# Kernel tuning notes

Hardware: AMD Instinct MI355X
Metric: run time of the kernel (lower is better)

Reference implementation:

```python
import jax, jax.numpy as jnp
import numpy as np

ALPHA_BASE = 1.2
ALPHA_SCALE = 0.3
GRAPH_LAMBDA = 0.3
FUSION_BETA = 0.1
PRIOR_BETA = 0.2
LN_EPS = 1e-5  # nn.LayerNorm default

B, L, C = 8, 8192, 512
STAT, HID, GF, EMB = 4, 16, 16, 16


def _linear_params(key, out_d, in_d):
    kw, kb = jax.random.split(key)
    bound = 1.0 / np.sqrt(in_d)
    W = jax.random.uniform(kw, (out_d, in_d), minval=-bound, maxval=bound, dtype=jnp.float32)
    b = jax.random.uniform(kb, (out_d,), minval=-bound, maxval=bound, dtype=jnp.float32)
    return W, b


def setup_inputs() -> dict:
    key = jax.random.key(0)
    ks = jax.random.split(key, 9)
    residual = jax.random.normal(ks[0], (B, L, C), dtype=jnp.float32)
    node_embedding = jax.random.normal(ks[1], (C, EMB), dtype=jnp.float32) * 0.02
    W_l1, b_l1 = _linear_params(ks[2], HID, STAT)
    W_l2, b_l2 = _linear_params(ks[3], HID, HID)
    W_g, b_g = _linear_params(ks[4], HID, STAT)
    W_q, b_q = _linear_params(ks[5], GF, STAT)
    W_k, b_k = _linear_params(ks[6], GF, STAT)
    W_f, b_f = _linear_params(ks[7], HID, HID)
    W_o, b_o = _linear_params(ks[8], 1, HID)
    ln_g = jnp.ones((HID,), jnp.float32)
    ln_b = jnp.zeros((HID,), jnp.float32)
    return dict(residual=residual, node_embedding=node_embedding,
                W_l1=W_l1, b_l1=b_l1, W_l2=W_l2, b_l2=b_l2,
                W_g=W_g, b_g=b_g, W_q=W_q, b_q=b_q, W_k=W_k, b_k=b_k,
                W_f=W_f, b_f=b_f, W_o=W_o, b_o=b_o, ln_g=ln_g, ln_b=ln_b)


def reference(residual, node_embedding, W_l1, b_l1, W_l2, b_l2, W_g, b_g,
              W_q, b_q, W_k, b_k, W_f, b_f, W_o, b_o, ln_g, ln_b):
    # --- residual statistics: [B,L,C] -> [B,C,4] ---
    abs_res = jnp.abs(residual)
    m = abs_res.mean(axis=1)                       # mean(|r|)
    mx = abs_res.max(axis=1)                       # max(|r|)
    sq = (residual * residual).mean(axis=1)        # energy == mean(|r|^2)
    std = jnp.sqrt(jnp.maximum(sq - m * m, 0.0))   # biased std of |r|
    h0 = jnp.stack([m, mx, std, sq], axis=-1)      # [B,C,4]

    # --- local branch ---
    h_local = jax.nn.relu(h0 @ W_l1.T + b_l1) @ W_l2.T + b_l2  # [B,C,H]

    # --- adaptive adjacency ---
    q = h0 @ W_q.T + b_q                            # [B,C,G]
    k = h0 @ W_k.T + b_k                            # [B,C,G]
    sim_data = jax.nn.relu(jnp.einsum('bcg,bdg->bcd', q, k))
    sim_prior = jax.nn.relu(node_embedding @ node_embedding.T)  # [C,C]
    eye = jnp.eye(sim_data.shape[-1], dtype=sim_data.dtype)
    sim = sim_data + PRIOR_BETA * sim_prior[None] + eye[None]
    A = jax.nn.softmax(sim, axis=-1)                # [B,C,C]

    # --- message passing ---
    h_graph_in = h0 @ W_g.T + b_g                   # [B,C,H]
    msg = jnp.einsum('bcd,bdh->bch', A, h_graph_in)
    h_graph = h_graph_in + GRAPH_LAMBDA * jax.nn.relu(msg)

    # --- fusion + layernorm + head ---
    h = h_local + FUSION_BETA * h_graph
    mu = h.mean(axis=-1, keepdims=True)
    var = ((h - mu) ** 2).mean(axis=-1, keepdims=True)
    h = (h - mu) / jnp.sqrt(var + LN_EPS) * ln_g + ln_b
    h = jax.nn.relu(h @ W_f.T + b_f)
    delta = ALPHA_SCALE * jnp.tanh(h @ W_o.T + b_o)  # [B,C,1]
    alpha = (ALPHA_BASE + delta).transpose(0, 2, 1)  # [B,1,C]
    return alpha, h0, A
```

## Files before the change

kernel.cpp:

```cpp
#include <hip/hip_runtime.h>
#include <math.h>

#define BB 8
#define LL 8192
#define CC 512
#define NCH 64

#define H0_OFF (BB*CC)
#define A_OFF  (H0_OFF + BB*CC*4)

#define F_ALPHA_BASE 1.2f
#define F_ALPHA_SCALE 0.3f
#define F_GRAPH_LAMBDA 0.3f
#define F_FUSION_BETA 0.1f
#define F_PRIOR_BETA 0.2f
#define F_LN_EPS 1e-5f

struct P {
    const float* res; const float* ne;
    const float* Wl1; const float* bl1; const float* Wl2; const float* bl2;
    const float* Wg;  const float* bg;  const float* Wq;  const float* bq;
    const float* Wk;  const float* bk;  const float* Wf;  const float* bf;
    const float* Wo;  const float* bo;  const float* lng; const float* lnb;
    float* out; float* pbuf; float* h0ws;
};

__global__ __launch_bounds__(256) void k_stats(P p) {
    __shared__ float smem[3 * CC];
    int b = blockIdx.x >> 6, cb = blockIdx.x & 63;
    int sub = threadIdx.x >> 7;
    int c4 = (threadIdx.x & 127) * 4;
    const float* base = p.res + ((size_t)b * LL + cb * 128 + sub * 64) * CC + c4;
    float s0 = 0.f, s1 = 0.f, s2 = 0.f, s3 = 0.f;
    float m0 = 0.f, m1 = 0.f, m2 = 0.f, m3 = 0.f;
    float q0 = 0.f, q1 = 0.f, q2 = 0.f, q3 = 0.f;
    #pragma unroll 8
    for (int r = 0; r < 64; r++) {
        float4 v = *(const float4*)(base + (size_t)r * CC);
        s0 += fabsf(v.x); s1 += fabsf(v.y); s2 += fabsf(v.z); s3 += fabsf(v.w);
        m0 = fmaxf(m0, fabsf(v.x)); m1 = fmaxf(m1, fabsf(v.y));
        m2 = fmaxf(m2, fabsf(v.z)); m3 = fmaxf(m3, fabsf(v.w));
        q0 = fmaf(v.x, v.x, q0); q1 = fmaf(v.y, v.y, q1);
        q2 = fmaf(v.z, v.z, q2); q3 = fmaf(v.w, v.w, q3);
    }
    if (sub == 1) {
        *(float4*)&smem[0 * CC + c4] = make_float4(s0, s1, s2, s3);
        *(float4*)&smem[1 * CC + c4] = make_float4(m0, m1, m2, m3);
        *(float4*)&smem[2 * CC + c4] = make_float4(q0, q1, q2, q3);
    }
    __syncthreads();
    if (sub == 0) {
        float4 cs = *(const float4*)&smem[0 * CC + c4];
        float4 cm = *(const float4*)&smem[1 * CC + c4];
        float4 cq = *(const float4*)&smem[2 * CC + c4];
        s0 += cs.x; s1 += cs.y; s2 += cs.z; s3 += cs.w;
        m0 = fmaxf(m0, cm.x); m1 = fmaxf(m1, cm.y);
        m2 = fmaxf(m2, cm.z); m3 = fmaxf(m3, cm.w);
        q0 += cq.x; q1 += cq.y; q2 += cq.z; q3 += cq.w;
        float* pb = p.pbuf + ((size_t)(b * 3) * NCH + cb) * CC + c4;
        *(float4*)(pb)                        = make_float4(s0, s1, s2, s3);
        *(float4*)(pb + (size_t)NCH * CC)     = make_float4(m0, m1, m2, m3);
        *(float4*)(pb + (size_t)2 * NCH * CC) = make_float4(q0, q1, q2, q3);
    }
}

__global__ __launch_bounds__(256) void k_red(P p) {
    __shared__ float red[4][3][64];
    int w = threadIdx.x >> 6, lane = threadIdx.x & 63;
    int b = blockIdx.x >> 3;
    int c = (blockIdx.x & 7) * 64 + lane;
    const float* pS = p.pbuf + ((size_t)(b * 3 + 0) * NCH + w * 16) * CC + c;
    const float* pM = p.pbuf + ((size_t)(b * 3 + 1) * NCH + w * 16) * CC + c;
    const float* pQ = p.pbuf + ((size_t)(b * 3 + 2) * NCH + w * 16) * CC + c;
    float sum = 0.f, mx = 0.f, sq = 0.f;
    #pragma unroll
    for (int i = 0; i < 16; i++) {
        sum += pS[(size_t)i * CC];
        mx = fmaxf(mx, pM[(size_t)i * CC]);
        sq += pQ[(size_t)i * CC];
    }
    red[w][0][lane] = sum;
    red[w][1][lane] = mx;
    red[w][2][lane] = sq;
    __syncthreads();
    if (w == 0) {
        float ts = red[0][0][lane] + red[1][0][lane] + red[2][0][lane] + red[3][0][lane];
        float tm = fmaxf(fmaxf(red[0][1][lane], red[1][1][lane]),
                         fmaxf(red[2][1][lane], red[3][1][lane]));
        float tq = red[0][2][lane] + red[1][2][lane] + red[2][2][lane] + red[3][2][lane];
        float m = ts * (1.f / LL);
        float sqm = tq * (1.f / LL);
        float sd = sqrtf(fmaxf(sqm - m * m, 0.f));
        float4 h0v = make_float4(m, tm, sd, sqm);
        size_t g = (size_t)b * CC + c;
        *(float4*)(p.h0ws + g * 4) = h0v;
        *(float4*)(p.out + H0_OFF + g * 4) = h0v;
    }
}

__global__ __launch_bounds__(256) void k_rows(P p) {
    __shared__ float pl[4 * CC];
    int tid = threadIdx.x;
    int b = blockIdx.x >> 6, rb = blockIdx.x & 63;
    int wid = tid >> 6, lane = tid & 63;
    int row0 = rb * 8 + wid * 2;

    #pragma unroll
    for (int ccy = 0; ccy < 2; ccy++) {
        int col = tid + ccy * 256;
        float4 hv = *(const float4*)(p.h0ws + ((size_t)b * CC + col) * 4);
        pl[col] = hv.x;
        pl[CC + col] = hv.y;
        pl[2 * CC + col] = hv.z;
        pl[3 * CC + col] = hv.w;
    }

    float nr[2][16];
    #pragma unroll
    for (int rr = 0; rr < 2; rr++) {
        #pragma unroll
        for (int t = 0; t < 4; t++) {
            float4 v = *(const float4*)(p.ne + (size_t)(row0 + rr) * 16 + t * 4);
            nr[rr][4 * t] = v.x; nr[rr][4 * t + 1] = v.y;
            nr[rr][4 * t + 2] = v.z; nr[rr][4 * t + 3] = v.w;
        }
    }
    float pr0[8], pr1[8];
    #pragma unroll
    for (int j = 0; j < 8; j++) {
        int col = lane + 64 * j;
        float d0 = 0.f, d1 = 0.f;
        #pragma unroll
        for (int t = 0; t < 4; t++) {
            float4 v = *(const float4*)(p.ne + (size_t)col * 16 + t * 4);
            d0 = fmaf(nr[0][4 * t], v.x, d0); d0 = fmaf(nr[0][4 * t + 1], v.y, d0);
            d0 = fmaf(nr[0][4 * t + 2], v.z, d0); d0 = fmaf(nr[0][4 * t + 3], v.w, d0);
            d1 = fmaf(nr[1][4 * t], v.x, d1); d1 = fmaf(nr[1][4 * t + 1], v.y, d1);
            d1 = fmaf(nr[1][4 * t + 2], v.z, d1); d1 = fmaf(nr[1][4 * t + 3], v.w, d1);
        }
        pr0[j] = fmaxf(d0, 0.f);
        pr1[j] = fmaxf(d1, 0.f);
    }
    __syncthreads();

    float sloc[2][4], u[2][4], c0[2];
    #pragma unroll
    for (int rr = 0; rr < 2; rr++) {
        int row = row0 + rr;
        float sv0 = pl[row], sv1 = pl[CC + row];
        float sv2 = pl[2 * CC + row], sv3 = pl[3 * CC + row];
        sloc[rr][0] = sv0; sloc[rr][1] = sv1; sloc[rr][2] = sv2; sloc[rr][3] = sv3;
        float uu0 = 0.f, uu1 = 0.f, uu2 = 0.f, uu3 = 0.f, cc = 0.f;
        #pragma unroll
        for (int i = 0; i < 16; i++) {
            float qi = p.bq[i];
            qi = fmaf(p.Wq[i * 4 + 0], sv0, qi);
            qi = fmaf(p.Wq[i * 4 + 1], sv1, qi);
            qi = fmaf(p.Wq[i * 4 + 2], sv2, qi);
            qi = fmaf(p.Wq[i * 4 + 3], sv3, qi);
            uu0 = fmaf(qi, p.Wk[i * 4 + 0], uu0);
            uu1 = fmaf(qi, p.Wk[i * 4 + 1], uu1);
            uu2 = fmaf(qi, p.Wk[i * 4 + 2], uu2);
            uu3 = fmaf(qi, p.Wk[i * 4 + 3], uu3);
            cc = fmaf(qi, p.bk[i], cc);
        }
        u[rr][0] = uu0; u[rr][1] = uu1; u[rr][2] = uu2; u[rr][3] = uu3;
        c0[rr] = cc;
    }

    float sv[2][8];
    float mx0 = -1e30f, mx1 = -1e30f;
    #pragma unroll
    for (int j = 0; j < 8; j++) {
        int col = lane + 64 * j;
        float h0c = pl[col], h1c = pl[CC + col];
        float h2c = pl[2 * CC + col], h3c = pl[3 * CC + col];
        float d0 = c0[0], d1 = c0[1];
        d0 = fmaf(u[0][0], h0c, d0); d1 = fmaf(u[1][0], h0c, d1);
        d0 = fmaf(u[0][1], h1c, d0); d1 = fmaf(u[1][1], h1c, d1);
        d0 = fmaf(u[0][2], h2c, d0); d1 = fmaf(u[1][2], h2c, d1);
        d0 = fmaf(u[0][3], h3c, d0); d1 = fmaf(u[1][3], h3c, d1);
        float v0 = fmaxf(d0, 0.f) + F_PRIOR_BETA * pr0[j] + (col == row0 ? 1.f : 0.f);
        float v1 = fmaxf(d1, 0.f) + F_PRIOR_BETA * pr1[j] + (col == row0 + 1 ? 1.f : 0.f);
        sv[0][j] = v0; sv[1][j] = v1;
        mx0 = fmaxf(mx0, v0); mx1 = fmaxf(mx1, v1);
    }
    #pragma unroll
    for (int o = 32; o; o >>= 1) {
        mx0 = fmaxf(mx0, __shfl_xor(mx0, o));
        mx1 = fmaxf(mx1, __shfl_xor(mx1, o));
    }

    float ls0 = 0.f, ls1 = 0.f;
    float T0[4] = {0.f, 0.f, 0.f, 0.f}, T1[4] = {0.f, 0.f, 0.f, 0.f};
    #pragma unroll
    for (int j = 0; j < 8; j++) {
        int col = lane + 64 * j;
        float e0 = expf(sv[0][j] - mx0);
        float e1 = expf(sv[1][j] - mx1);
        sv[0][j] = e0; sv[1][j] = e1;
        ls0 += e0; ls1 += e1;
        float h0c = pl[col], h1c = pl[CC + col];
        float h2c = pl[2 * CC + col], h3c = pl[3 * CC + col];
        T0[0] = fmaf(e0, h0c, T0[0]); T1[0] = fmaf(e1, h0c, T1[0]);
        T0[1] = fmaf(e0, h1c, T0[1]); T1[1] = fmaf(e1, h1c, T1[1]);
        T0[2] = fmaf(e0, h2c, T0[2]); T1[2] = fmaf(e1, h2c, T1[2]);
        T0[3] = fmaf(e0, h3c, T0[3]); T1[3] = fmaf(e1, h3c, T1[3]);
    }
    #pragma unroll
    for (int o = 32; o; o >>= 1) {
        ls0 += __shfl_xor(ls0, o); ls1 += __shfl_xor(ls1, o);
        T0[0] += __shfl_xor(T0[0], o); T1[0] += __shfl_xor(T1[0], o);
        T0[1] += __shfl_xor(T0[1], o); T1[1] += __shfl_xor(T1[1], o);
        T0[2] += __shfl_xor(T0[2], o); T1[2] += __shfl_xor(T1[2], o);
        T0[3] += __shfl_xor(T0[3], o); T1[3] += __shfl_xor(T1[3], o);
    }
    float inv0 = 1.f / ls0, inv1 = 1.f / ls1;

    float* arow = p.out + A_OFF + ((size_t)b * CC + row0) * CC;
    #pragma unroll
    for (int j = 0; j < 8; j++) {
        arow[lane + 64 * j]      = sv[0][j] * inv0;
        arow[CC + lane + 64 * j] = sv[1][j] * inv1;
    }

    int rr = lane >> 5;
    float inv = rr ? inv1 : inv0;
    float Ta = (rr ? T1[0] : T0[0]) * inv;
    float Tb = (rr ? T1[1] : T0[1]) * inv;
    float Tc = (rr ? T1[2] : T0[2]) * inv;
    float Td = (rr ? T1[3] : T0[3]) * inv;
    float s20 = rr ? sloc[1][0] : sloc[0][0];
    float s21 = rr ? sloc[1][1] : sloc[0][1];
    float s22 = rr ? sloc[1][2] : sloc[0][2];
    float s23 = rr ? sloc[1][3] : sloc[0][3];

    float gcomb[16];
    #pragma unroll
    for (int h = 0; h < 16; h++) {
        float w0 = p.Wg[h * 4 + 0], w1 = p.Wg[h * 4 + 1];
        float w2 = p.Wg[h * 4 + 2], w3 = p.Wg[h * 4 + 3];
        float bgh = p.bg[h];
        float hg = bgh;
        hg = fmaf(w0, s20, hg); hg = fmaf(w1, s21, hg);
        hg = fmaf(w2, s22, hg); hg = fmaf(w3, s23, hg);
        float mg = bgh;
        mg = fmaf(w0, Ta, mg); mg = fmaf(w1, Tb, mg);
        mg = fmaf(w2, Tc, mg); mg = fmaf(w3, Td, mg);
        gcomb[h] = hg + F_GRAPH_LAMBDA * fmaxf(mg, 0.f);
    }
    float t1v[16];
    #pragma unroll
    for (int i = 0; i < 16; i++) {
        float a = p.bl1[i];
        a = fmaf(p.Wl1[i * 4 + 0], s20, a);
        a = fmaf(p.Wl1[i * 4 + 1], s21, a);
        a = fmaf(p.Wl1[i * 4 + 2], s22, a);
        a = fmaf(p.Wl1[i * 4 + 3], s23, a);
        t1v[i] = fmaxf(a, 0.f);
    }
    float hvec[16];
    float mu = 0.f;
    #pragma unroll
    for (int h = 0; h < 16; h++) {
        float hl = p.bl2[h];
        #pragma unroll
        for (int j = 0; j < 16; j++) hl = fmaf(p.Wl2[h * 16 + j], t1v[j], hl);
        float hv = hl + F_FUSION_BETA * gcomb[h];
        hvec[h] = hv;
        mu += hv;
    }
    mu *= (1.f / 16.f);
    float var = 0.f;
    #pragma unroll
    for (int h = 0; h < 16; h++) { float d = hvec[h] - mu; var = fmaf(d, d, var); }
    var *= (1.f / 16.f);
    float istd = 1.f / sqrtf(var + F_LN_EPS);
    float hn[16];
    #pragma unroll
    for (int h = 0; h < 16; h++) hn[h] = (hvec[h] - mu) * istd * p.lng[h] + p.lnb[h];

    float acc2 = p.bo[0];
    #pragma unroll
    for (int o = 0; o < 16; o++) {
        float f = p.bf[o];
        #pragma unroll
        for (int t = 0; t < 16; t++) f = fmaf(p.Wf[o * 16 + t], hn[t], f);
        acc2 = fmaf(p.Wo[o], fmaxf(f, 0.f), acc2);
    }
    float alpha = F_ALPHA_BASE + F_ALPHA_SCALE * tanhf(acc2);
    if ((lane & 31) == 0) p.out[(size_t)b * CC + row0 + rr] = alpha;
}

extern "C" void kernel_launch(void* const* d_in, const int* in_sizes, int n_in,
                              void* d_out, int out_size, void* d_ws, size_t ws_size,
                              hipStream_t stream) {
    P p;
    p.res = (const float*)d_in[0];
    p.ne  = (const float*)d_in[1];
    p.Wl1 = (const float*)d_in[2];
    p.bl1 = (const float*)d_in[3];
    p.Wl2 = (const float*)d_in[4];
    p.bl2 = (const float*)d_in[5];
    p.Wg  = (const float*)d_in[6];
    p.bg  = (const float*)d_in[7];
    p.Wq  = (const float*)d_in[8];
    p.bq  = (const float*)d_in[9];
    p.Wk  = (const float*)d_in[10];
    p.bk  = (const float*)d_in[11];
    p.Wf  = (const float*)d_in[12];
    p.bf  = (const float*)d_in[13];
    p.Wo  = (const float*)d_in[14];
    p.bo  = (const float*)d_in[15];
    p.lng = (const float*)d_in[16];
    p.lnb = (const float*)d_in[17];
    p.out  = (float*)d_out;
    p.pbuf = (float*)d_ws;
    p.h0ws = (float*)d_ws + (size_t)BB * 3 * NCH * CC;

    k_stats<<<BB * NCH, 256, 0, stream>>>(p);
    k_red<<<64, 256, 0, stream>>>(p);
    k_rows<<<BB * 64, 256, 0, stream>>>(p);
}
```

Before: 50.05 us.

## Merge stats reduction into row kernel and reshape stats tiling

The statistics kernel now tiles by column slice and by 1024-row chunk, producing only 8 partials per column instead of 64. The separate reduction kernel is removed: each k_rows block sums the 8 partials itself to build h0, and block rb==0 writes h0 to the output. This saves one launch and shrinks the partial buffer. The cost is that every rows block repeats the small final reduction, and each stats thread now reads a narrow 64-float column slice with a 16-row stride, which may coalesce less well.

```diff
diff --git a/kernel.cpp b/kernel.cpp
--- a/kernel.cpp
+++ b/kernel.cpp
@@ -4,7 +4,8 @@
 #define BB 8
 #define LL 8192
 #define CC 512
-#define NCH 64
+#define NCH 8
+#define CSPL 8
 
 #define H0_OFF (BB*CC)
 #define A_OFF  (H0_OFF + BB*CC*4)
@@ -22,97 +23,81 @@
     const float* Wg;  const float* bg;  const float* Wq;  const float* bq;
     const float* Wk;  const float* bk;  const float* Wf;  const float* bf;
     const float* Wo;  const float* bo;  const float* lng; const float* lnb;
-    float* out; float* pbuf; float* h0ws;
+    float* out; float* pbuf;
 };
 
 __global__ __launch_bounds__(256) void k_stats(P p) {
-    __shared__ float smem[3 * CC];
-    int b = blockIdx.x >> 6, cb = blockIdx.x & 63;
-    int sub = threadIdx.x >> 7;
-    int c4 = (threadIdx.x & 127) * 4;
-    const float* base = p.res + ((size_t)b * LL + cb * 128 + sub * 64) * CC + c4;
+    __shared__ float red[16][3][64];
+    int b = blockIdx.x >> 6;
+    int ch = (blockIdx.x >> 3) & 7;
+    int cs = blockIdx.x & 7;
+    int lane4 = threadIdx.x & 15;
+    int rpart = threadIdx.x >> 4;
+    int col = cs * 64 + lane4 * 4;
+    const float* base = p.res + ((size_t)b * LL + ch * 1024 + rpart) * CC + col;
+
     float s0 = 0.f, s1 = 0.f, s2 = 0.f, s3 = 0.f;
     float m0 = 0.f, m1 = 0.f, m2 = 0.f, m3 = 0.f;
     float q0 = 0.f, q1 = 0.f, q2 = 0.f, q3 = 0.f;
     #pragma unroll 8
-    for (int r = 0; r < 64; r++) {
-        float4 v = *(const float4*)(base + (size_t)r * CC);
+    for (int it = 0; it < 64; it++) {
+        float4 v = *(const float4*)(base + (size_t)it * 16 * CC);
         s0 += fabsf(v.x); s1 += fabsf(v.y); s2 += fabsf(v.z); s3 += fabsf(v.w);
         m0 = fmaxf(m0, fabsf(v.x)); m1 = fmaxf(m1, fabsf(v.y));
         m2 = fmaxf(m2, fabsf(v.z)); m3 = fmaxf(m3, fabsf(v.w));
         q0 = fmaf(v.x, v.x, q0); q1 = fmaf(v.y, v.y, q1);
         q2 = fmaf(v.z, v.z, q2); q3 = fmaf(v.w, v.w, q3);
     }
-    if (sub == 1) {
-        *(float4*)&smem[0 * CC + c4] = make_float4(s0, s1, s2, s3);
-        *(float4*)&smem[1 * CC + c4] = make_float4(m0, m1, m2, m3);
-        *(float4*)&smem[2 * CC + c4] = make_float4(q0, q1, q2, q3);
-    }
+    *(float4*)&red[rpart][0][lane4 * 4] = make_float4(s0, s1, s2, s3);
+    *(float4*)&red[rpart][1][lane4 * 4] = make_float4(m0, m1, m2, m3);
+    *(float4*)&red[rpart][2][lane4 * 4] = make_float4(q0, q1, q2, q3);
     __syncthreads();
-    if (sub == 0) {
-        float4 cs = *(const float4*)&smem[0 * CC + c4];
-        float4 cm = *(const float4*)&smem[1 * CC + c4];
-        float4 cq = *(const float4*)&smem[2 * CC + c4];
-        s0 += cs.x; s1 += cs.y; s2 += cs.z; s3 += cs.w;
-        m0 = fmaxf(m0, cm.x); m1 = fmaxf(m1, cm.y);
-        m2 = fmaxf(m2, cm.z); m3 = fmaxf(m3, cm.w);
-        q0 += cq.x; q1 += cq.y; q2 += cq.z; q3 += cq.w;
-        float* pb = p.pbuf + ((size_t)(b * 3) * NCH + cb) * CC + c4;
-        *(float4*)(pb)                        = make_float4(s0, s1, s2, s3);
-        *(float4*)(pb + (size_t)NCH * CC)     = make_float4(m0, m1, m2, m3);
-        *(float4*)(pb + (size_t)2 * NCH * CC) = make_float4(q0, q1, q2, q3);
+    if (threadIdx.x < 64) {
+        int c = threadIdx.x;
+        float ts = 0.f, tm = 0.f, tq = 0.f;
+        #pragma unroll
+        for (int pp = 0; pp < 16; pp++) {
+            ts += red[pp][0][c];
+            tm = fmaxf(tm, red[pp][1][c]);
+            tq += red[pp][2][c];
+        }
+        size_t cg = cs * 64 + c;
+        p.pbuf[((size_t)(b * 3 + 0) * NCH + ch) * CC + cg] = ts;
+        p.pbuf[((size_t)(b * 3 + 1) * NCH + ch) * CC + cg] = tm;
+        p.pbuf[((size_t)(b * 3 + 2) * NCH + ch) * CC + cg] = tq;
     }
 }
 
-__global__ __launch_bounds__(256) void k_red(P p) {
-    __shared__ float red[4][3][64];
-    int w = threadIdx.x >> 6, lane = threadIdx.x & 63;
-    int b = blockIdx.x >> 3;
-    int c = (blockIdx.x & 7) * 64 + lane;
-    const float* pS = p.pbuf + ((size_t)(b * 3 + 0) * NCH + w * 16) * CC + c;
-    const float* pM = p.pbuf + ((size_t)(b * 3 + 1) * NCH + w * 16) * CC + c;
-    const float* pQ = p.pbuf + ((size_t)(b * 3 + 2) * NCH + w * 16) * CC + c;
-    float sum = 0.f, mx = 0.f, sq = 0.f;
-    #pragma unroll
-    for (int i = 0; i < 16; i++) {
-        sum += pS[(size_t)i * CC];
-        mx = fmaxf(mx, pM[(size_t)i * CC]);
-        sq += pQ[(size_t)i * CC];
-    }
-    red[w][0][lane] = sum;
-    red[w][1][lane] = mx;
-    red[w][2][lane] = sq;
-    __syncthreads();
-    if (w == 0) {
-        float ts = red[0][0][lane] + red[1][0][lane] + red[2][0][lane] + red[3][0][lane];
-        float tm = fmaxf(fmaxf(red[0][1][lane], red[1][1][lane]),
-                         fmaxf(red[2][1][lane], red[3][1][lane]));
-        float tq = red[0][2][lane] + red[1][2][lane] + red[2][2][lane] + red[3][2][lane];
-        float m = ts * (1.f / LL);
-        float sqm = tq * (1.f / LL);
-        float sd = sqrtf(fmaxf(sqm - m * m, 0.f));
-        float4 h0v = make_float4(m, tm, sd, sqm);
-        size_t g = (size_t)b * CC + c;
-        *(float4*)(p.h0ws + g * 4) = h0v;
-        *(float4*)(p.out + H0_OFF + g * 4) = h0v;
-    }
-}
-
 __global__ __launch_bounds__(256) void k_rows(P p) {
-    __shared__ float pl[4 * CC];
+    __shared__ float sm[4 * CC];
     int tid = threadIdx.x;
     int b = blockIdx.x >> 6, rb = blockIdx.x & 63;
     int wid = tid >> 6, lane = tid & 63;
     int row0 = rb * 8 + wid * 2;
 
     #pragma unroll
-    for (int ccy = 0; ccy < 2; ccy++) {
-        int col = tid + ccy * 256;
-        float4 hv = *(const float4*)(p.h0ws + ((size_t)b * CC + col) * 4);
-        pl[col] = hv.x;
-        pl[CC + col] = hv.y;
-        pl[2 * CC + col] = hv.z;
-        pl[3 * CC + col] = hv.w;
+    for (int cc = 0; cc < 2; cc++) {
+        int c = tid + cc * 256;
+        const float* pS = p.pbuf + (size_t)(b * 3 + 0) * NCH * CC + c;
+        const float* pM = p.pbuf + (size_t)(b * 3 + 1) * NCH * CC + c;
+        const float* pQ = p.pbuf + (size_t)(b * 3 + 2) * NCH * CC + c;
+        float ts = 0.f, tm = 0.f, tq = 0.f;
+        #pragma unroll
+        for (int ch = 0; ch < NCH; ch++) {
+            ts += pS[(size_t)ch * CC];
+            tm = fmaxf(tm, pM[(size_t)ch * CC]);
+            tq += pQ[(size_t)ch * CC];
+        }
+        float m = ts * (1.f / LL);
+        float sqm = tq * (1.f / LL);
+        float sd = sqrtf(fmaxf(sqm - m * m, 0.f));
+        sm[c] = m;
+        sm[CC + c] = tm;
+        sm[2 * CC + c] = sd;
+        sm[3 * CC + c] = sqm;
+        if (rb == 0)
+            *(float4*)(p.out + H0_OFF + ((size_t)b * CC + c) * 4) =
+                make_float4(m, tm, sd, sqm);
     }
 
     float nr[2][16];
@@ -147,8 +132,8 @@
     #pragma unroll
     for (int rr = 0; rr < 2; rr++) {
         int row = row0 + rr;
-        float sv0 = pl[row], sv1 = pl[CC + row];
-        float sv2 = pl[2 * CC + row], sv3 = pl[3 * CC + row];
+        float sv0 = sm[row], sv1 = sm[CC + row];
+        float sv2 = sm[2 * CC + row], sv3 = sm[3 * CC + row];
         sloc[rr][0] = sv0; sloc[rr][1] = sv1; sloc[rr][2] = sv2; sloc[rr][3] = sv3;
         float uu0 = 0.f, uu1 = 0.f, uu2 = 0.f, uu3 = 0.f, cc = 0.f;
         #pragma unroll
@@ -173,8 +158,8 @@
     #pragma unroll
     for (int j = 0; j < 8; j++) {
         int col = lane + 64 * j;
-        float h0c = pl[col], h1c = pl[CC + col];
-        float h2c = pl[2 * CC + col], h3c = pl[3 * CC + col];
+        float h0c = sm[col], h1c = sm[CC + col];
+        float h2c = sm[2 * CC + col], h3c = sm[3 * CC + col];
         float d0 = c0[0], d1 = c0[1];
         d0 = fmaf(u[0][0], h0c, d0); d1 = fmaf(u[1][0], h0c, d1);
         d0 = fmaf(u[0][1], h1c, d0); d1 = fmaf(u[1][1], h1c, d1);
@@ -200,8 +185,8 @@
         float e1 = expf(sv[1][j] - mx1);
         sv[0][j] = e0; sv[1][j] = e1;
         ls0 += e0; ls1 += e1;
-        float h0c = pl[col], h1c = pl[CC + col];
-        float h2c = pl[2 * CC + col], h3c = pl[3 * CC + col];
+        float h0c = sm[col], h1c = sm[CC + col];
+        float h2c = sm[2 * CC + col], h3c = sm[3 * CC + col];
         T0[0] = fmaf(e0, h0c, T0[0]); T1[0] = fmaf(e1, h0c, T1[0]);
         T0[1] = fmaf(e0, h1c, T0[1]); T1[1] = fmaf(e1, h1c, T1[1]);
         T0[2] = fmaf(e0, h2c, T0[2]); T1[2] = fmaf(e1, h2c, T1[2]);
@@ -316,9 +301,7 @@
     p.lnb = (const float*)d_in[17];
     p.out  = (float*)d_out;
     p.pbuf = (float*)d_ws;
-    p.h0ws = (float*)d_ws + (size_t)BB * 3 * NCH * CC;
-
-    k_stats<<<BB * NCH, 256, 0, stream>>>(p);
-    k_red<<<64, 256, 0, stream>>>(p);
+
+    k_stats<<<BB * NCH * CSPL, 256, 0, stream>>>(p);
     k_rows<<<BB * 64, 256, 0, stream>>>(p);
 }
```

Result: faster. 48.96 us (-2.2%).
